# Performance work log

Measured on AMD Instinct MI355X. Metric: run time of the kernel, lower is better.

## Reference

```python
import jax, jax.numpy as jnp
import numpy as np

EPS = 1e-8

def _l2norm(x):
    # normalize rows, guarding against zero norm like torch cosine similarity eps
    n = jnp.sqrt(jnp.sum(x * x, axis=-1, keepdims=True))
    return x / jnp.maximum(n, EPS)

def setup_inputs() -> dict:
    key = jax.random.key(0)
    k1, k2, k3 = jax.random.split(key, 3)
    Nq, Nk, D = 4096, 4096, 1024
    return {
        "queries": jax.random.normal(k1, (Nq, D), dtype=jnp.float32),
        "keys": jax.random.normal(k2, (Nk, D), dtype=jnp.float32),
        "values": jax.random.normal(k3, (Nk, D), dtype=jnp.float32),
    }

def reference(queries, keys, values):
    # CosineSimilarityMatrix(keys, queries): [Nk, Nq] pairwise cosine sims
    attn_weights = jnp.matmul(_l2norm(keys), _l2norm(queries).T)  # [Nk, Nq]
    # weighted sum over keys for each query
    weighted = jnp.matmul(attn_weights.T, values)  # [Nq, D]
    return (weighted, attn_weights)
```

## Files before the change

### kernel.cpp

```cpp
#include <hip/hip_runtime.h>


typedef unsigned short u16;
typedef unsigned int u32;
typedef float f32x4 __attribute__((ext_vector_type(4)));
typedef __bf16 bf16x8 __attribute__((ext_vector_type(8)));

__device__ __forceinline__ u16 f2bf(float f) {
  u32 u = __builtin_bit_cast(u32, f);
  return (u16)((u + 0x7FFFu + ((u >> 16) & 1u)) >> 16);
}

__device__ __forceinline__ void gload16(const u16* g, u16* l) {
  void* gp = (void*)g;
  void* lp = (void*)l;
  __builtin_amdgcn_global_load_lds((__attribute__((address_space(1))) void*)gp,
                                   (__attribute__((address_space(3))) void*)lp, 16, 0, 0);
}

#define BARRIER() __builtin_amdgcn_s_barrier()
#define WAITVM(n) asm volatile("s_waitcnt vmcnt(" #n ")" ::: "memory")
#define WAITLGKM0() do { asm volatile("s_waitcnt lgkmcnt(0)" ::: "memory"); \
                         __builtin_amdgcn_sched_barrier(0); } while (0)

__global__ __launch_bounds__(256) void norm_transv_kernel(
    const float* __restrict__ q, const float* __restrict__ k,
    u16* __restrict__ qnb, u16* __restrict__ knb,
    const float* __restrict__ v, u16* __restrict__ vbT) {
  int bid = blockIdx.x, t = threadIdx.x;
  if (bid < 8192) {
    const float* src = (bid < 4096) ? q : k;
    u16* dst = (bid < 4096) ? qnb : knb;
    int row = bid & 4095;
    const float4 val = ((const float4*)(src + (size_t)row * 1024))[t];
    float s = val.x * val.x + val.y * val.y + val.z * val.z + val.w * val.w;
    #pragma unroll
    for (int off = 32; off > 0; off >>= 1) s += __shfl_xor(s, off, 64);
    __shared__ float red[4];
    if ((t & 63) == 0) red[t >> 6] = s;
    __syncthreads();
    float inv = 1.0f / fmaxf(sqrtf(red[0] + red[1] + red[2] + red[3]), 1e-8f);
    uint2 o;
    o.x = (u32)f2bf(val.x * inv) | ((u32)f2bf(val.y * inv) << 16);
    o.y = (u32)f2bf(val.z * inv) | ((u32)f2bf(val.w * inv) << 16);
    *(uint2*)(dst + (size_t)row * 1024 + t * 4) = o;
  } else {
    __shared__ __align__(16) float lds[64 * 64];
    int tix = bid - 8192;
    int r0 = (tix >> 4) * 64, c0 = (tix & 15) * 64;
    int ch = t & 15, lr = t >> 4;
    #pragma unroll
    for (int i = 0; i < 4; ++i) {
      int r = lr + i * 16;
      float4 val = *(const float4*)&v[(size_t)(r0 + r) * 1024 + c0 + ch * 4];
      int byteoff = r * 256 + ((ch * 16) ^ (((r >> 3) & 7) << 4));
      *(float4*)((char*)lds + byteoff) = val;
    }
    __syncthreads();
    int cch = t & 7, lrow = t >> 3;
    #pragma unroll
    for (int i = 0; i < 2; ++i) {
      int oc = lrow + i * 32;
      u16 vals[8];
      #pragma unroll
      for (int j = 0; j < 8; ++j) {
        int srl = cch * 8 + j;
        int byteoff = srl * 256 + (((oc >> 2) * 16) ^ (((srl >> 3) & 7) << 4)) + (oc & 3) * 4;
        vals[j] = f2bf(*(const float*)((const char*)lds + byteoff));
      }
      uint4 o;
      o.x = (u32)vals[0] | ((u32)vals[1] << 16);
      o.y = (u32)vals[2] | ((u32)vals[3] << 16);
      o.z = (u32)vals[4] | ((u32)vals[5] << 16);
      o.w = (u32)vals[6] | ((u32)vals[7] << 16);
      *(uint4*)&vbT[(size_t)(c0 + oc) * 4096 + r0 + cch * 8] = o;
    }
  }
}

__global__ __launch_bounds__(256) void transpose_bf16_kernel(
    const u16* __restrict__ src, u16* __restrict__ dst) {
  int b = blockIdx.x;
  int r0 = (b >> 4) * 64, c0 = (b & 15) * 64;
  __shared__ __align__(16) u16 lds[64 * 64];
  int t = threadIdx.x;
  int lrow = t >> 3, cch = t & 7;
  #pragma unroll
  for (int i = 0; i < 2; ++i) {
    int sr = lrow + i * 32;
    uint4 val = *(const uint4*)&src[(size_t)(r0 + sr) * 1024 + c0 + cch * 8];
    int byteoff = sr * 128 + ((cch * 16) ^ (((sr >> 3) & 7) << 4));
    *(uint4*)((char*)lds + byteoff) = val;
  }
  __syncthreads();
  #pragma unroll
  for (int i = 0; i < 2; ++i) {
    int oc = lrow + i * 32;
    u16 vals[8];
    #pragma unroll
    for (int j = 0; j < 8; ++j) {
      int srl = cch * 8 + j;
      int byteoff = srl * 128 + ((oc * 2) ^ (cch << 4));
      vals[j] = *(const u16*)((const char*)lds + byteoff);
    }
    uint4 o;
    o.x = (u32)vals[0] | ((u32)vals[1] << 16);
    o.y = (u32)vals[2] | ((u32)vals[3] << 16);
    o.z = (u32)vals[4] | ((u32)vals[5] << 16);
    o.w = (u32)vals[6] | ((u32)vals[7] << 16);
    *(uint4*)&dst[(size_t)(c0 + oc) * 4096 + r0 + cch * 8] = o;
  }
}

template<int BM, int BN, int MW, int NW>
__global__ __launch_bounds__(256) void gemm_abt(
    const u16* __restrict__ A, const u16* __restrict__ B, float* __restrict__ Cptr,
    int k_len, int lda, int ldb, int ldc, int plane) {
  static_assert(BM == 2 * MW * 16 && BN == 2 * NW * 16, "wave grid is 2x2");
  __shared__ __align__(16) u16 ldsA[2][BM * 64];
  __shared__ __align__(16) u16 ldsB[2][BN * 64];
  const int t = threadIdx.x, l = t & 63, w = t >> 6;
  const int tileM = blockIdx.y, tileN = blockIdx.x;
  const int k_start = blockIdx.z * k_len;
  Cptr += (size_t)blockIdx.z * plane;
  const int srow = l >> 3, schunk = (l & 7) * 8;
  const u16* gA = A + (size_t)(tileM * BM) * lda + k_start + schunk;
  const u16* gB = B + (size_t)(tileN * BN) * ldb + k_start + schunk;
  const int aoff = ((w >> 1) * MW * 16 + (l & 15)) * 64 + (l >> 4) * 8;
  const int boff = ((w & 1) * NW * 16 + (l & 15)) * 64 + (l >> 4) * 8;

  f32x4 acc[MW][NW];
  #pragma unroll
  for (int m = 0; m < MW; ++m)
    #pragma unroll
    for (int n = 0; n < NW; ++n) acc[m][n] = (f32x4){0.f, 0.f, 0.f, 0.f};

  auto stage = [&](int buf, int kof) {
    #pragma unroll
    for (int j = 0; j < BM / 32; ++j) {
      const int r = w * (BM / 4) + j * 8;
      gload16(gA + (size_t)(r + srow) * lda + kof, &ldsA[buf][r * 64]);
    }
    #pragma unroll
    for (int j = 0; j < BN / 32; ++j) {
      const int r = w * (BN / 4) + j * 8;
      gload16(gB + (size_t)(r + srow) * ldb + kof, &ldsB[buf][r * 64]);
    }
  };

  bf16x8 av0[MW], bv0[NW], av1[MW], bv1[NW];
  const int nt = k_len >> 6;
  stage(0, 0);
  __syncthreads();
  #pragma unroll
  for (int m = 0; m < MW; ++m) av0[m] = *(const bf16x8*)&ldsA[0][aoff + m * 16 * 64];
  #pragma unroll
  for (int n = 0; n < NW; ++n) bv0[n] = *(const bf16x8*)&ldsB[0][boff + n * 16 * 64];

  for (int i = 0; i < nt; ++i) {
    const int cur = i & 1;
    if (i + 1 < nt) stage(cur ^ 1, (i + 1) * 64);
    #pragma unroll
    for (int m = 0; m < MW; ++m) av1[m] = *(const bf16x8*)&ldsA[cur][aoff + m * 16 * 64 + 32];
    #pragma unroll
    for (int n = 0; n < NW; ++n) bv1[n] = *(const bf16x8*)&ldsB[cur][boff + n * 16 * 64 + 32];
    #pragma unroll
    for (int m = 0; m < MW; ++m)
      #pragma unroll
      for (int n = 0; n < NW; ++n)
        acc[m][n] = __builtin_amdgcn_mfma_f32_16x16x32_bf16(av0[m], bv0[n], acc[m][n], 0, 0, 0);
    #pragma unroll
    for (int m = 0; m < MW; ++m)
      #pragma unroll
      for (int n = 0; n < NW; ++n)
        acc[m][n] = __builtin_amdgcn_mfma_f32_16x16x32_bf16(av1[m], bv1[n], acc[m][n], 0, 0, 0);
    __syncthreads();
    if (i + 1 < nt) {
      const int nxt = cur ^ 1;
      #pragma unroll
      for (int m = 0; m < MW; ++m) av0[m] = *(const bf16x8*)&ldsA[nxt][aoff + m * 16 * 64];
      #pragma unroll
      for (int n = 0; n < NW; ++n) bv0[n] = *(const bf16x8*)&ldsB[nxt][boff + n * 16 * 64];
    }
  }

  const int orow = tileM * BM + (w >> 1) * MW * 16 + (l >> 4) * 4;
  const int ocol = tileN * BN + (w & 1) * NW * 16 + (l & 15);
  #pragma unroll
  for (int m = 0; m < MW; ++m)
    #pragma unroll
    for (int n = 0; n < NW; ++n)
      #pragma unroll
      for (int r = 0; r < 4; ++r)
        Cptr[(size_t)(orow + m * 16 + r) * ldc + (ocol + n * 16)] = acc[m][n][r];
}

__global__ __launch_bounds__(512, 2) void gemm256_abt(
    const u16* __restrict__ A, const u16* __restrict__ B, float* __restrict__ C,
    const float* __restrict__ P, u16* __restrict__ ctred,
    int K, int lda, int ldb, int ldc, int ntn) {
  __shared__ __align__(16) u16 lds[65536];
  const int tid = threadIdx.x, l = tid & 63, w = tid >> 6;
  const int wm = w >> 2, wn = w & 3;
  const int nwg = gridDim.x * gridDim.y;
  const int bid = blockIdx.y * gridDim.x + blockIdx.x;
  const int swz = (bid & 7) * (nwg >> 3) + (bid >> 3);
  const int tileM = swz / ntn, tileN = swz % ntn;

  const int q0 = w * 128 + l, q1 = q0 + 64;
  const int r0 = q0 >> 2, r1 = q1 >> 2;
  const int s0 = ((q0 & 3) ^ ((r0 >> 1) & 3)) << 3;
  const int s1 = ((q1 & 3) ^ ((r1 >> 1) & 3)) << 3;
  const int d0 = w * 1024, d1 = d0 + 512;
  const u16* gA = A + (size_t)tileM * 256 * lda;
  const u16* gB = B + (size_t)tileN * 256 * ldb;
  const int offA0 = r0 * lda + s0, offA1 = r1 * lda + s1;
  const int offB0 = r0 * ldb + s0, offB1 = r1 * ldb + s1;

#define STGA(kof, dst) do { gload16(gA + (kof) + offA0, lds + (dst) + d0); \
                            gload16(gA + (kof) + offA1, lds + (dst) + d1); } while (0)
#define STGB(kof, dst) do { gload16(gB + (kof) + offB0, lds + (dst) + d0); \
                            gload16(gB + (kof) + offB1, lds + (dst) + d1); } while (0)
  const int NT = K >> 6;
  STGA(0, 0);
  STGB(0, 16384);
  STGA(32, 8192);
  STGB(32, 24576);
  STGA(64, 32768);
  STGB(64, 32768 + 16384);
  {
    const int base = bid * 4096 + tid * 8;
    f32x4 sa = *(const f32x4*)&P[base];
    f32x4 sb = *(const f32x4*)&P[base + 4];
    #pragma unroll
    for (int p = 1; p < 4; ++p) {
      sa += *(const f32x4*)&P[(size_t)p * 1048576 + base];
      sb += *(const f32x4*)&P[(size_t)p * 1048576 + base + 4];
    }
    uint4 o;
    o.x = (u32)f2bf(sa[0]) | ((u32)f2bf(sa[1]) << 16);
    o.y = (u32)f2bf(sa[2]) | ((u32)f2bf(sa[3]) << 16);
    o.z = (u32)f2bf(sb[0]) | ((u32)f2bf(sb[1]) << 16);
    o.w = (u32)f2bf(sb[2]) | ((u32)f2bf(sb[3]) << 16);
    *(uint4*)&ctred[base] = o;
  }
  WAITVM(8);
  BARRIER();

  const int scol = (((l >> 4) ^ ((l >> 1) & 3)) << 3);
  const int afrag = (wm * 128 + (l & 15)) * 32 + scol;
  const int bfrag = (wn * 64 + (l & 15)) * 32 + scol;

  f32x4 acc[8][4];
  #pragma unroll
  for (int m = 0; m < 8; ++m)
    #pragma unroll
    for (int n = 0; n < 4; ++n) acc[m][n] = (f32x4){0.f, 0.f, 0.f, 0.f};

#define MFMA_BLK(AV, BV, MB) do { \
    __builtin_amdgcn_s_setprio(1); \
    _Pragma("unroll") \
    for (int m = 0; m < 4; ++m) { \
      _Pragma("unroll") \
      for (int n = 0; n < 4; ++n) \
        acc[(MB) + m][n] = __builtin_amdgcn_mfma_f32_16x16x32_bf16(AV[m], BV[n], acc[(MB) + m][n], 0, 0, 0); \
    } \
    __builtin_amdgcn_s_setprio(0); } while (0)

  bf16x8 A0[4], A1[4], B0[4], B1[4];
  #pragma unroll
  for (int m = 0; m < 4; ++m) A0[m] = *(const bf16x8*)&lds[afrag + m * 512];
  #pragma unroll
  for (int n = 0; n < 4; ++n) B0[n] = *(const bf16x8*)&lds[16384 + bfrag + n * 512];

  for (int t = 0; t < NT; ++t) {
    const int co = (t & 1) << 15, no = co ^ 32768;
    const u16* bufc = lds + co;
    const u16* bufn = lds + no;
    const int koff = t * 64;
    if (t + 1 < NT) STGA(koff + 96, no + 8192);
    #pragma unroll
    for (int m = 0; m < 4; ++m) A1[m] = *(const bf16x8*)&bufc[afrag + (m + 4) * 512];
    BARRIER();
    WAITLGKM0();
    MFMA_BLK(A0, B0, 0);
    if (t + 1 < NT) { WAITVM(6); } else { WAITVM(0); }
    BARRIER();
    if (t + 1 < NT) STGB(koff + 96, no + 24576);
    #pragma unroll
    for (int m = 0; m < 4; ++m) A0[m] = *(const bf16x8*)&bufc[8192 + afrag + m * 512];
    #pragma unroll
    for (int n = 0; n < 4; ++n) B1[n] = *(const bf16x8*)&bufc[24576 + bfrag + n * 512];
    BARRIER();
    WAITLGKM0();
    MFMA_BLK(A1, B0, 4);
    BARRIER();
    if (t + 2 < NT) STGA(koff + 128, co);
    #pragma unroll
    for (int m = 0; m < 4; ++m) A1[m] = *(const bf16x8*)&bufc[8192 + afrag + (m + 4) * 512];
    BARRIER();
    WAITLGKM0();
    MFMA_BLK(A0, B1, 0);
    BARRIER();
    if (t + 2 < NT) STGB(koff + 128, co + 16384);
    BARRIER();
    WAITLGKM0();
    MFMA_BLK(A1, B1, 4);
    if (t + 1 < NT) {
      if (t + 2 < NT) { WAITVM(8); } else { WAITVM(4); }
    }
    BARRIER();
    if (t + 1 < NT) {
      #pragma unroll
      for (int m = 0; m < 4; ++m) A0[m] = *(const bf16x8*)&bufn[afrag + m * 512];
      #pragma unroll
      for (int n = 0; n < 4; ++n) B0[n] = *(const bf16x8*)&bufn[16384 + bfrag + n * 512];
    }
  }

  const int orow = tileM * 256 + wm * 128 + (l >> 4) * 4;
  const int ocol = tileN * 256 + wn * 64 + (l & 15);
  #pragma unroll
  for (int m = 0; m < 8; ++m)
    #pragma unroll
    for (int n = 0; n < 4; ++n)
      #pragma unroll
      for (int r = 0; r < 4; ++r)
        C[(size_t)(orow + m * 16 + r) * ldc + (ocol + n * 16)] = acc[m][n][r];
#undef STGA
#undef STGB
#undef MFMA_BLK
}

extern "C" void kernel_launch(void* const* d_in, const int* in_sizes, int n_in,
                              void* d_out, int out_size, void* d_ws, size_t ws_size,
                              hipStream_t stream) {
  const float* q = (const float*)d_in[0];
  const float* k = (const float*)d_in[1];
  const float* v = (const float*)d_in[2];
  float* out = (float*)d_out;
  float* weighted = out;
  float* attn = out + 4194304;

  char* ws = (char*)d_ws;
  u16* qnb = (u16*)(ws);
  u16* knb = (u16*)(ws + (8u << 20));
  u16* knT = (u16*)(ws + (16u << 20));
  u16* vbT = (u16*)(ws + (24u << 20));
  u16* ct  = (u16*)(ws + (32u << 20));

  norm_transv_kernel<<<9216, 256, 0, stream>>>(q, k, qnb, knb, v, vbT);
  transpose_bf16_kernel<<<1024, 256, 0, stream>>>(knb, knT);
  gemm_abt<128, 64, 4, 2><<<dim3(16, 8, 4), 256, 0, stream>>>(
      vbT, knT, weighted, 1024, 4096, 4096, 1024, 1048576);
  gemm256_abt<<<dim3(16, 16), 512, 0, stream>>>(
      knb, qnb, attn, weighted, ct, 1024, 1024, 1024, 4096, 16);
  gemm_abt<128, 64, 4, 2><<<dim3(16, 32, 1), 256, 0, stream>>>(
      qnb, ct, weighted, 1024, 1024, 1024, 1024, 0);
}
```

Before: 99.35 us.

## Compute attention-weight GEMM in int8 with per-row scales and deeper pipeline

The normalization kernel now also writes int8-quantized copies of the normalized queries and keys, with one scale per row. The large Nk×Nq cosine GEMM now uses i8 MFMA (16x16x64) on these copies and applies the two row scales during the output store. Its LDS staging is rebuilt into a 4-stage ring of 64-wide K chunks. This halves operand bytes and doubles the MFMA K-depth per instruction, at the cost of int8 quantization error in attn_weights, which may exceed tolerance, and a larger LDS footprint (128KB) that could limit occupancy.

```diff
diff --git a/kernel.cpp b/kernel.cpp
--- a/kernel.cpp
+++ b/kernel.cpp
@@ -3,7 +3,9 @@
 
 typedef unsigned short u16;
 typedef unsigned int u32;
+typedef unsigned char u8;
 typedef float f32x4 __attribute__((ext_vector_type(4)));
+typedef int int4v __attribute__((ext_vector_type(4)));
 typedef __bf16 bf16x8 __attribute__((ext_vector_type(8)));
 
 __device__ __forceinline__ u16 f2bf(float f) {
@@ -12,10 +14,12 @@
 }
 
 __device__ __forceinline__ void gload16(const u16* g, u16* l) {
-  void* gp = (void*)g;
-  void* lp = (void*)l;
-  __builtin_amdgcn_global_load_lds((__attribute__((address_space(1))) void*)gp,
-                                   (__attribute__((address_space(3))) void*)lp, 16, 0, 0);
+  __builtin_amdgcn_global_load_lds((__attribute__((address_space(1))) void*)(void*)g,
+                                   (__attribute__((address_space(3))) void*)(void*)l, 16, 0, 0);
+}
+__device__ __forceinline__ void gload16b(const u8* g, u8* l) {
+  __builtin_amdgcn_global_load_lds((__attribute__((address_space(1))) void*)(void*)g,
+                                   (__attribute__((address_space(3))) void*)(void*)l, 16, 0, 0);
 }
 
 #define BARRIER() __builtin_amdgcn_s_barrier()
@@ -26,24 +30,45 @@
 __global__ __launch_bounds__(256) void norm_transv_kernel(
     const float* __restrict__ q, const float* __restrict__ k,
     u16* __restrict__ qnb, u16* __restrict__ knb,
+    u8* __restrict__ qnq, u8* __restrict__ knq,
+    float* __restrict__ sclQ, float* __restrict__ sclK,
     const float* __restrict__ v, u16* __restrict__ vbT) {
   int bid = blockIdx.x, t = threadIdx.x;
   if (bid < 8192) {
-    const float* src = (bid < 4096) ? q : k;
-    u16* dst = (bid < 4096) ? qnb : knb;
+    const bool isQ = (bid < 4096);
+    const float* src = isQ ? q : k;
+    u16* dst = isQ ? qnb : knb;
+    u8* dst8 = isQ ? qnq : knq;
+    float* scl = isQ ? sclQ : sclK;
     int row = bid & 4095;
     const float4 val = ((const float4*)(src + (size_t)row * 1024))[t];
     float s = val.x * val.x + val.y * val.y + val.z * val.z + val.w * val.w;
-    #pragma unroll
-    for (int off = 32; off > 0; off >>= 1) s += __shfl_xor(s, off, 64);
-    __shared__ float red[4];
-    if ((t & 63) == 0) red[t >> 6] = s;
+    float am = fmaxf(fmaxf(fabsf(val.x), fabsf(val.y)), fmaxf(fabsf(val.z), fabsf(val.w)));
+    #pragma unroll
+    for (int off = 32; off > 0; off >>= 1) {
+      s += __shfl_xor(s, off, 64);
+      am = fmaxf(am, __shfl_xor(am, off, 64));
+    }
+    __shared__ float2 red[4];
+    if ((t & 63) == 0) red[t >> 6] = make_float2(s, am);
     __syncthreads();
-    float inv = 1.0f / fmaxf(sqrtf(red[0] + red[1] + red[2] + red[3]), 1e-8f);
+    float tot = red[0].x + red[1].x + red[2].x + red[3].x;
+    float amall = fmaxf(fmaxf(red[0].y, red[1].y), fmaxf(red[2].y, red[3].y));
+    float inv = 1.0f / fmaxf(sqrtf(tot), 1e-8f);
+    float rm = fmaxf(amall * inv, 1e-30f);
+    float iq = 127.0f / rm;
     uint2 o;
     o.x = (u32)f2bf(val.x * inv) | ((u32)f2bf(val.y * inv) << 16);
     o.y = (u32)f2bf(val.z * inv) | ((u32)f2bf(val.w * inv) << 16);
     *(uint2*)(dst + (size_t)row * 1024 + t * 4) = o;
+    int c0 = (int)rintf(val.x * inv * iq);
+    int c1 = (int)rintf(val.y * inv * iq);
+    int c2 = (int)rintf(val.z * inv * iq);
+    int c3 = (int)rintf(val.w * inv * iq);
+    u32 p = (u32)(c0 & 255) | ((u32)(c1 & 255) << 8) |
+            ((u32)(c2 & 255) << 16) | ((u32)(c3 & 255) << 24);
+    ((u32*)(dst8 + (size_t)row * 1024))[t] = p;
+    if (t == 0) scl[row] = rm * (1.0f / 127.0f);
   } else {
     __shared__ __align__(16) float lds[64 * 64];
     int tix = bid - 8192;
@@ -195,11 +220,11 @@
         Cptr[(size_t)(orow + m * 16 + r) * ldc + (ocol + n * 16)] = acc[m][n][r];
 }
 
-__global__ __launch_bounds__(512, 2) void gemm256_abt(
-    const u16* __restrict__ A, const u16* __restrict__ B, float* __restrict__ C,
+__global__ __launch_bounds__(512, 2) void gemm256_i8(
+    const u8* __restrict__ A8, const u8* __restrict__ B8, float* __restrict__ C,
     const float* __restrict__ P, u16* __restrict__ ctred,
-    int K, int lda, int ldb, int ldc, int ntn) {
-  __shared__ __align__(16) u16 lds[65536];
+    const float* __restrict__ sclK, const float* __restrict__ sclQ, int ntn) {
+  __shared__ __align__(16) u8 lds8[131072];
   const int tid = threadIdx.x, l = tid & 63, w = tid >> 6;
   const int wm = w >> 2, wn = w & 3;
   const int nwg = gridDim.x * gridDim.y;
@@ -207,27 +232,23 @@
   const int swz = (bid & 7) * (nwg >> 3) + (bid >> 3);
   const int tileM = swz / ntn, tileN = swz % ntn;
 
-  const int q0 = w * 128 + l, q1 = q0 + 64;
-  const int r0 = q0 >> 2, r1 = q1 >> 2;
-  const int s0 = ((q0 & 3) ^ ((r0 >> 1) & 3)) << 3;
-  const int s1 = ((q1 & 3) ^ ((r1 >> 1) & 3)) << 3;
-  const int d0 = w * 1024, d1 = d0 + 512;
-  const u16* gA = A + (size_t)tileM * 256 * lda;
-  const u16* gB = B + (size_t)tileN * 256 * ldb;
-  const int offA0 = r0 * lda + s0, offA1 = r1 * lda + s1;
-  const int offB0 = r0 * ldb + s0, offB1 = r1 * ldb + s1;
-
-#define STGA(kof, dst) do { gload16(gA + (kof) + offA0, lds + (dst) + d0); \
-                            gload16(gA + (kof) + offA1, lds + (dst) + d1); } while (0)
-#define STGB(kof, dst) do { gload16(gB + (kof) + offB0, lds + (dst) + d0); \
-                            gload16(gB + (kof) + offB1, lds + (dst) + d1); } while (0)
-  const int NT = K >> 6;
-  STGA(0, 0);
-  STGB(0, 16384);
-  STGA(32, 8192);
-  STGB(32, 24576);
-  STGA(64, 32768);
-  STGB(64, 32768 + 16384);
+  const int r0 = w * 32 + (l >> 2);
+  const int s0 = ((l & 3) ^ ((l >> 3) & 3)) * 16;
+  const int offA = r0 * 1024 + s0;
+  const u8* gA8 = A8 + (size_t)tileM * 256 * 1024;
+  const u8* gB8 = B8 + (size_t)tileN * 256 * 1024;
+
+#define STGA8(kof, bb) do { \
+    gload16b(gA8 + (kof) + offA,          lds8 + (bb) + w * 2048); \
+    gload16b(gA8 + (kof) + offA + 16384,  lds8 + (bb) + w * 2048 + 1024); } while (0)
+#define STGB8(kof, bb) do { \
+    gload16b(gB8 + (kof) + offA,          lds8 + (bb) + 16384 + w * 2048); \
+    gload16b(gB8 + (kof) + offA + 16384,  lds8 + (bb) + 16384 + w * 2048 + 1024); } while (0)
+
+  STGA8(0, 0);        STGB8(0, 0);
+  STGA8(64, 32768);   STGB8(64, 32768);
+  STGA8(128, 65536);  STGB8(128, 65536);
+  STGA8(192, 98304);  STGB8(192, 98304);
   {
     const int base = bid * 4096 + tid * 8;
     f32x4 sa = *(const f32x4*)&P[base];
@@ -244,92 +265,80 @@
     o.w = (u32)f2bf(sb[2]) | ((u32)f2bf(sb[3]) << 16);
     *(uint4*)&ctred[base] = o;
   }
-  WAITVM(8);
+  WAITVM(0);
   BARRIER();
 
-  const int scol = (((l >> 4) ^ ((l >> 1) & 3)) << 3);
-  const int afrag = (wm * 128 + (l & 15)) * 32 + scol;
-  const int bfrag = (wn * 64 + (l & 15)) * 32 + scol;
-
-  f32x4 acc[8][4];
+  const int scol = ((l >> 4) ^ ((l >> 1) & 3)) * 16;
+  const int afragB = (wm * 128 + (l & 15)) * 64 + scol;
+  const int bfragB = (wn * 64 + (l & 15)) * 64 + scol;
+
+  int4v acc[8][4];
   #pragma unroll
   for (int m = 0; m < 8; ++m)
     #pragma unroll
-    for (int n = 0; n < 4; ++n) acc[m][n] = (f32x4){0.f, 0.f, 0.f, 0.f};
-
-#define MFMA_BLK(AV, BV, MB) do { \
-    __builtin_amdgcn_s_setprio(1); \
-    _Pragma("unroll") \
-    for (int m = 0; m < 4; ++m) { \
-      _Pragma("unroll") \
-      for (int n = 0; n < 4; ++n) \
-        acc[(MB) + m][n] = __builtin_amdgcn_mfma_f32_16x16x32_bf16(AV[m], BV[n], acc[(MB) + m][n], 0, 0, 0); \
-    } \
-    __builtin_amdgcn_s_setprio(0); } while (0)
-
-  bf16x8 A0[4], A1[4], B0[4], B1[4];
-  #pragma unroll
-  for (int m = 0; m < 4; ++m) A0[m] = *(const bf16x8*)&lds[afrag + m * 512];
-  #pragma unroll
-  for (int n = 0; n < 4; ++n) B0[n] = *(const bf16x8*)&lds[16384 + bfrag + n * 512];
-
+    for (int n = 0; n < 4; ++n) acc[m][n] = (int4v){0, 0, 0, 0};
+
+  int4v A0[4], A1[4], B0[4];
+  #pragma unroll
+  for (int m = 0; m < 4; ++m) A0[m] = *(const int4v*)&lds8[afragB + m * 1024];
+  #pragma unroll
+  for (int n = 0; n < 4; ++n) B0[n] = *(const int4v*)&lds8[16384 + bfragB + n * 1024];
+
+  const int NT = 16;
   for (int t = 0; t < NT; ++t) {
-    const int co = (t & 1) << 15, no = co ^ 32768;
-    const u16* bufc = lds + co;
-    const u16* bufn = lds + no;
+    const int bb = (t & 3) * 32768;
     const int koff = t * 64;
-    if (t + 1 < NT) STGA(koff + 96, no + 8192);
-    #pragma unroll
-    for (int m = 0; m < 4; ++m) A1[m] = *(const bf16x8*)&bufc[afrag + (m + 4) * 512];
+    #pragma unroll
+    for (int m = 0; m < 4; ++m) A1[m] = *(const int4v*)&lds8[bb + afragB + (m + 4) * 1024];
     BARRIER();
     WAITLGKM0();
-    MFMA_BLK(A0, B0, 0);
-    if (t + 1 < NT) { WAITVM(6); } else { WAITVM(0); }
+    __builtin_amdgcn_s_setprio(1);
+    #pragma unroll
+    for (int m = 0; m < 4; ++m)
+      #pragma unroll
+      for (int n = 0; n < 4; ++n)
+        acc[m][n] = __builtin_amdgcn_mfma_i32_16x16x64_i8(A0[m], B0[n], acc[m][n], 0, 0, 0);
+    __builtin_amdgcn_s_setprio(0);
     BARRIER();
-    if (t + 1 < NT) STGB(koff + 96, no + 24576);
-    #pragma unroll
-    for (int m = 0; m < 4; ++m) A0[m] = *(const bf16x8*)&bufc[8192 + afrag + m * 512];
-    #pragma unroll
-    for (int n = 0; n < 4; ++n) B1[n] = *(const bf16x8*)&bufc[24576 + bfrag + n * 512];
-    BARRIER();
-    WAITLGKM0();
-    MFMA_BLK(A1, B0, 4);
-    BARRIER();
-    if (t + 2 < NT) STGA(koff + 128, co);
-    #pragma unroll
-    for (int m = 0; m < 4; ++m) A1[m] = *(const bf16x8*)&bufc[8192 + afrag + (m + 4) * 512];
-    BARRIER();
-    WAITLGKM0();
-    MFMA_BLK(A0, B1, 0);
-    BARRIER();
-    if (t + 2 < NT) STGB(koff + 128, co + 16384);
-    BARRIER();
-    WAITLGKM0();
-    MFMA_BLK(A1, B1, 4);
-    if (t + 1 < NT) {
-      if (t + 2 < NT) { WAITVM(8); } else { WAITVM(4); }
-    }
+    if (t + 4 < NT) { STGA8(koff + 256, bb); STGB8(koff + 256, bb); }
+    __builtin_amdgcn_s_setprio(1);
+    #pragma unroll
+    for (int m = 0; m < 4; ++m)
+      #pragma unroll
+      for (int n = 0; n < 4; ++n)
+        acc[m + 4][n] = __builtin_amdgcn_mfma_i32_16x16x64_i8(A1[m], B0[n], acc[m + 4][n], 0, 0, 0);
+    __builtin_amdgcn_s_setprio(0);
+    if (t + 4 < NT)      { WAITVM(12); }
+    else if (t + 3 < NT) { WAITVM(8); }
+    else if (t + 2 < NT) { WAITVM(4); }
+    else if (t + 1 < NT) { WAITVM(0); }
     BARRIER();
     if (t + 1 < NT) {
-      #pragma unroll
-      for (int m = 0; m < 4; ++m) A0[m] = *(const bf16x8*)&bufn[afrag + m * 512];
-      #pragma unroll
-      for (int n = 0; n < 4; ++n) B0[n] = *(const bf16x8*)&bufn[16384 + bfrag + n * 512];
+      const int nb = ((t + 1) & 3) * 32768;
+      #pragma unroll
+      for (int m = 0; m < 4; ++m) A0[m] = *(const int4v*)&lds8[nb + afragB + m * 1024];
+      #pragma unroll
+      for (int n = 0; n < 4; ++n) B0[n] = *(const int4v*)&lds8[nb + 16384 + bfragB + n * 1024];
     }
   }
 
   const int orow = tileM * 256 + wm * 128 + (l >> 4) * 4;
   const int ocol = tileN * 256 + wn * 64 + (l & 15);
-  #pragma unroll
-  for (int m = 0; m < 8; ++m)
+  float sq[4];
+  #pragma unroll
+  for (int n = 0; n < 4; ++n) sq[n] = sclQ[ocol + n * 16];
+  #pragma unroll
+  for (int m = 0; m < 8; ++m) {
+    const float4 sk4 = *(const float4*)&sclK[orow + m * 16];
     #pragma unroll
     for (int n = 0; n < 4; ++n)
       #pragma unroll
       for (int r = 0; r < 4; ++r)
-        C[(size_t)(orow + m * 16 + r) * ldc + (ocol + n * 16)] = acc[m][n][r];
-#undef STGA
-#undef STGB
-#undef MFMA_BLK
+        C[(size_t)(orow + m * 16 + r) * 4096 + (ocol + n * 16)] =
+            (float)acc[m][n][r] * ((const float*)&sk4)[r] * sq[n];
+  }
+#undef STGA8
+#undef STGB8
 }
 
 extern "C" void kernel_launch(void* const* d_in, const int* in_sizes, int n_in,
@@ -348,13 +357,17 @@
   u16* knT = (u16*)(ws + (16u << 20));
   u16* vbT = (u16*)(ws + (24u << 20));
   u16* ct  = (u16*)(ws + (32u << 20));
-
-  norm_transv_kernel<<<9216, 256, 0, stream>>>(q, k, qnb, knb, v, vbT);
+  u8*  qnq = (u8*)(ws + (34u << 20));
+  u8*  knq = (u8*)(ws + (38u << 20));
+  float* sclQ = (float*)(ws + (42u << 20));
+  float* sclK = (float*)(ws + (42u << 20) + 65536);
+
+  norm_transv_kernel<<<9216, 256, 0, stream>>>(q, k, qnb, knb, qnq, knq, sclQ, sclK, v, vbT);
   transpose_bf16_kernel<<<1024, 256, 0, stream>>>(knb, knT);
   gemm_abt<128, 64, 4, 2><<<dim3(16, 8, 4), 256, 0, stream>>>(
       vbT, knT, weighted, 1024, 4096, 4096, 1024, 1048576);
-  gemm256_abt<<<dim3(16, 16), 512, 0, stream>>>(
-      knb, qnb, attn, weighted, ct, 1024, 1024, 1024, 4096, 16);
+  gemm256_i8<<<dim3(16, 16), 512, 0, stream>>>(
+      knq, qnq, attn, weighted, ct, sclK, sclQ, 16);
   gemm_abt<128, 64, 4, 2><<<dim3(16, 32, 1), 256, 0, stream>>>(
       qnb, ct, weighted, 1024, 1024, 1024, 1024, 0);
 }
```

Result: faster. 88.22 us (-11.2%).
